# Kernel optimization log

Measured on AMD Instinct MI355X. Metric: run time of the kernel, lower is better.

## Reference

```python
import jax, jax.numpy as jnp
import numpy as np

D = 128  # d_pair
N = 512  # n_res
B = 1
EPS = 1e-5


def setup_inputs() -> dict:
    key = jax.random.key(0)
    ks = jax.random.split(key, 16)
    s = 0.02
    inp = {
        "pair": jax.random.normal(ks[0], (B, N, N, D), dtype=jnp.float32),
        "pair_mask": jnp.ones((B, N, N), dtype=jnp.float32),
        "ln_g": jnp.ones((D,), dtype=jnp.float32),
        "ln_b": jnp.zeros((D,), dtype=jnp.float32),
        "w_lp": jax.random.normal(ks[1], (D, D), dtype=jnp.float32) * s,
        "b_lp": jnp.zeros((D,), dtype=jnp.float32),
        "w_lg": jax.random.normal(ks[2], (D, D), dtype=jnp.float32) * s,
        "b_lg": jnp.zeros((D,), dtype=jnp.float32),
        "w_rp": jax.random.normal(ks[3], (D, D), dtype=jnp.float32) * s,
        "b_rp": jnp.zeros((D,), dtype=jnp.float32),
        "w_rg": jax.random.normal(ks[4], (D, D), dtype=jnp.float32) * s,
        "b_rg": jnp.zeros((D,), dtype=jnp.float32),
        "w_g": jax.random.normal(ks[5], (D, D), dtype=jnp.float32) * s,
        "b_g": jnp.zeros((D,), dtype=jnp.float32),
        "w_o": jax.random.normal(ks[6], (D, D), dtype=jnp.float32) * s,
        "b_o": jnp.zeros((D,), dtype=jnp.float32),
    }
    return inp


def _layer_norm(x, g, b):
    mu = jnp.mean(x, axis=-1, keepdims=True)
    var = jnp.mean(jnp.square(x - mu), axis=-1, keepdims=True)
    return (x - mu) * jax.lax.rsqrt(var + EPS) * g + b


def reference(pair, pair_mask, ln_g, ln_b, w_lp, b_lp, w_lg, b_lg,
              w_rp, b_rp, w_rg, b_rg, w_g, b_g, w_o, b_o):
    # [B,N,N,D] pair representation; outgoing triangle multiplication
    x = _layer_norm(pair, ln_g, ln_b)
    mask = pair_mask[..., None]  # [B,N,N,1]
    left = (x @ w_lp + b_lp) * jax.nn.sigmoid(x @ w_lg + b_lg) * mask
    right = (x @ w_rp + b_rp) * jax.nn.sigmoid(x @ w_rg + b_rg) * mask
    # outgoing: contract over j -> per-channel NxN matmul
    out = jnp.einsum('bijd,bjkd->bikd', left, right)
    out = out * jax.nn.sigmoid(x @ w_g + b_g)
    out = out @ w_o + b_o
    return out
```

## Files before the change

### kernel.cpp

```cpp
#include <hip/hip_runtime.h>

#define NN 512
#define DD 128
#define PP (NN*NN)

typedef __attribute__((ext_vector_type(8))) short short8;
typedef __attribute__((ext_vector_type(4))) short shortx4;
typedef __attribute__((ext_vector_type(4))) float floatx4;

__device__ __forceinline__ unsigned short f2bf(float f) {
  unsigned int u = __float_as_uint(f);
  u += 0x7fffu + ((u >> 16) & 1u);
  return (unsigned short)(u >> 16);
}
__device__ __forceinline__ float bf2f(unsigned short h) {
  return __uint_as_float(((unsigned int)h) << 16);
}
__device__ __forceinline__ float sigm(float x) {
  return 1.f / (1.f + __expf(-x));
}

__device__ __forceinline__ void gload_lds16(const unsigned short* g, unsigned short* l) {
  __builtin_amdgcn_global_load_lds(
      (const __attribute__((address_space(1))) unsigned int*)g,
      (__attribute__((address_space(3))) unsigned int*)l, 16, 0, 0);
}

__global__ void k0_prep(const float* __restrict__ wlp, const float* __restrict__ wlg,
                        const float* __restrict__ wrp, const float* __restrict__ wrg,
                        const float* __restrict__ wg,  const float* __restrict__ wo,
                        unsigned short* __restrict__ wt) {
  const float* src[6] = {wlp, wlg, wrp, wrg, wg, wo};
  int m = blockIdx.y;
  int idx = blockIdx.x * 256 + threadIdx.x;
  int d = idx >> 7, e = idx & 127;
  wt[m * 16384 + e * 128 + d] = f2bf(src[m][d * 128 + e]);
}

__device__ __forceinline__ void run_mm(const unsigned short* __restrict__ wt_m,
                                       unsigned short* Alds, unsigned short* Wlds,
                                       int t, int wm, int we, int ln, int q8,
                                       floatx4 (&acc)[4][4]) {
  #pragma unroll
  for (int it = 0; it < 8; ++it) {
    int flat = it * 256 + t;
    int e = flat >> 4, c = flat & 15;
    *(short8*)&Wlds[e * 136 + c * 8] = *(const short8*)(wt_m + e * 128 + c * 8);
  }
  __syncthreads();
  #pragma unroll
  for (int ks = 0; ks < 4; ++ks) {
    short8 a[4], b[4];
    #pragma unroll
    for (int i = 0; i < 4; ++i)
      a[i] = *(const short8*)&Alds[(wm + i * 16 + ln) * 136 + ks * 32 + q8 * 8];
    #pragma unroll
    for (int i = 0; i < 4; ++i)
      b[i] = *(const short8*)&Wlds[(we + i * 16 + ln) * 136 + ks * 32 + q8 * 8];
    #pragma unroll
    for (int i = 0; i < 4; ++i)
      #pragma unroll
      for (int j = 0; j < 4; ++j)
        acc[i][j] = __builtin_amdgcn_mfma_f32_16x16x32_bf16(a[i], b[j], acc[i][j], 0, 0, 0);
  }
  __syncthreads();
}

__launch_bounds__(256, 2)
__global__ void k1_ln_proj(const float* __restrict__ pair, const float* __restrict__ pmask,
                           const float* __restrict__ lng, const float* __restrict__ lnb,
                           const unsigned short* __restrict__ wt,
                           const float* __restrict__ b_lp, const float* __restrict__ b_lg,
                           const float* __restrict__ b_rp, const float* __restrict__ b_rg,
                           const float* __restrict__ b_g,
                           unsigned short* __restrict__ left_t,
                           unsigned short* __restrict__ right_bt,
                           unsigned short* __restrict__ gate_t) {
  __shared__ __align__(16) unsigned short Alds[128 * 136];
  __shared__ __align__(16) unsigned short Wlds[128 * 136];
  __shared__ float Mlds[128];

  const int t = threadIdx.x;
  const int unit = blockIdx.y;
  const int q = blockIdx.x;

  long prow0, pstride, mrow0, mstride, soff;
  if (unit == 1) {
    int j0 = (q >> 9) << 7, k0 = q & 511;
    prow0 = ((long)j0 * NN + k0) * DD; pstride = (long)NN * DD;
    mrow0 = (long)j0 * NN + k0;        mstride = NN;
    soff  = (long)k0 * NN + j0;
  } else {
    long p0 = (long)q << 7;
    prow0 = p0 * DD; pstride = DD;
    mrow0 = p0;      mstride = 1;
    soff  = p0;
  }

  {
    int r = t >> 1, h = t & 1;
    const float* row = pair + prow0 + (long)r * pstride + h * 64;
    floatx4 v[16];
    float s = 0.f, s2 = 0.f;
    #pragma unroll
    for (int c = 0; c < 16; ++c) {
      v[c] = *(const floatx4*)(row + c * 4);
      s  += v[c].x + v[c].y + v[c].z + v[c].w;
      s2 += v[c].x * v[c].x + v[c].y * v[c].y + v[c].z * v[c].z + v[c].w * v[c].w;
    }
    s  += __shfl_xor(s, 1);
    s2 += __shfl_xor(s2, 1);
    float mu = s * (1.f / 128.f);
    float var = s2 * (1.f / 128.f) - mu * mu;
    float rs = rsqrtf(var + 1e-5f);
    #pragma unroll
    for (int c = 0; c < 16; ++c) {
      floatx4 g4 = *(const floatx4*)(lng + h * 64 + c * 4);
      floatx4 b4 = *(const floatx4*)(lnb + h * 64 + c * 4);
      shortx4 pk;
      pk[0] = (short)f2bf((v[c].x - mu) * rs * g4.x + b4.x);
      pk[1] = (short)f2bf((v[c].y - mu) * rs * g4.y + b4.y);
      pk[2] = (short)f2bf((v[c].z - mu) * rs * g4.z + b4.z);
      pk[3] = (short)f2bf((v[c].w - mu) * rs * g4.w + b4.w);
      *(shortx4*)&Alds[r * 136 + h * 64 + c * 4] = pk;
    }
    if (h == 0) Mlds[r] = pmask[mrow0 + (long)r * mstride];
  }
  __syncthreads();

  const int lane = t & 63, w = t >> 6;
  const int ln = lane & 15, q8 = lane >> 4;
  const int wm = (w >> 1) << 6, we = (w & 1) << 6;

  unsigned short* stg = (w < 2) ? (Alds + w * 4608) : (Wlds + (w - 2) * 4608);

  if (unit < 2) {
    floatx4 accA[4][4] = {};
    floatx4 accB[4][4] = {};
    run_mm(wt + (unit == 0 ? 0 : 2) * 16384, Alds, Wlds, t, wm, we, ln, q8, accA);
    run_mm(wt + (unit == 0 ? 1 : 3) * 16384, Alds, Wlds, t, wm, we, ln, q8, accB);
    const float* bpp = (unit == 0) ? b_lp : b_rp;
    const float* bgg = (unit == 0) ? b_lg : b_rg;
    #pragma unroll
    for (int j = 0; j < 4; ++j) {
      int eg = we + j * 16 + ln;
      float bp_v = bpp[eg], bg_v = bgg[eg];
      #pragma unroll
      for (int i = 0; i < 4; ++i) {
        shortx4 pk;
        #pragma unroll
        for (int r = 0; r < 4; ++r) {
          int m = wm + i * 16 + q8 * 4 + r;
          float val = (accA[i][j][r] + bp_v) * sigm(accB[i][j][r] + bg_v) * Mlds[m];
          pk[r] = (short)f2bf(val);
        }
        *(shortx4*)&stg[(j * 16 + ln) * 72 + i * 16 + q8 * 4] = pk;
      }
    }
  } else {
    floatx4 accA[4][4] = {};
    run_mm(wt + 4 * 16384, Alds, Wlds, t, wm, we, ln, q8, accA);
    #pragma unroll
    for (int j = 0; j < 4; ++j) {
      int eg = we + j * 16 + ln;
      float bg_v = b_g[eg];
      #pragma unroll
      for (int i = 0; i < 4; ++i) {
        shortx4 pk;
        #pragma unroll
        for (int r = 0; r < 4; ++r)
          pk[r] = (short)f2bf(sigm(accA[i][j][r] + bg_v));
        *(shortx4*)&stg[(j * 16 + ln) * 72 + i * 16 + q8 * 4] = pk;
      }
    }
  }
  __syncthreads();

  unsigned short* dstbase = (unit == 0) ? left_t : (unit == 1 ? right_bt : gate_t);
  #pragma unroll
  for (int itr = 0; itr < 8; ++itr) {
    int row = itr * 8 + (lane >> 3);
    int c = lane & 7;
    short8 vv = *(const short8*)&stg[row * 72 + c * 8];
    long eg = we + row;
    *(short8*)(dstbase + eg * PP + soff + wm + c * 8) = vv;
  }
}

__launch_bounds__(256, 3)
__global__ void k2_einsum(const unsigned short* __restrict__ left_t,
                          const unsigned short* __restrict__ right_bt,
                          const unsigned short* __restrict__ gate_t,
                          unsigned short* __restrict__ tmpg) {
  __shared__ __align__(16) unsigned short Al[128 * 32];
  __shared__ __align__(16) unsigned short Bl[128 * 32];
  const int t = threadIdx.x;
  const int d = blockIdx.y;
  const int i0 = (blockIdx.x >> 2) << 7;
  const int k0 = (blockIdx.x & 3) << 7;
  const unsigned short* Ag = left_t   + (long)d * PP;
  const unsigned short* Bg = right_bt + (long)d * PP;
  const int lane = t & 63, w = t >> 6;
  const int ln = lane & 15, q8 = lane >> 4;
  const int wm = (w >> 1) << 6, wn = (w & 1) << 6;

  floatx4 acc[4][4] = {};
  for (int j0 = 0; j0 < NN; j0 += 32) {
    #pragma unroll
    for (int it = 0; it < 2; ++it) {
      int flat = it * 256 + t;
      int r = flat >> 2, c = flat & 3;
      gload_lds16(Ag + (long)(i0 + r) * NN + j0 + c * 8, &Al[flat * 8]);
    }
    #pragma unroll
    for (int it = 0; it < 2; ++it) {
      int flat = it * 256 + t;
      int r = flat >> 2, c = flat & 3;
      gload_lds16(Bg + (long)(k0 + r) * NN + j0 + c * 8, &Bl[flat * 8]);
    }
    __syncthreads();
    short8 a[4], b[4];
    #pragma unroll
    for (int i = 0; i < 4; ++i)
      a[i] = *(const short8*)&Al[(wm + i * 16 + ln) * 32 + q8 * 8];
    #pragma unroll
    for (int i = 0; i < 4; ++i)
      b[i] = *(const short8*)&Bl[(wn + i * 16 + ln) * 32 + q8 * 8];
    #pragma unroll
    for (int i = 0; i < 4; ++i)
      #pragma unroll
      for (int j = 0; j < 4; ++j)
        acc[i][j] = __builtin_amdgcn_mfma_f32_16x16x32_bf16(a[i], b[j], acc[i][j], 0, 0, 0);
    __syncthreads();
  }
  const unsigned short* Gg = gate_t + (long)d * PP;
  unsigned short* Og = tmpg + (long)d * PP;
  #pragma unroll
  for (int i = 0; i < 4; ++i)
    #pragma unroll
    for (int j = 0; j < 4; ++j) {
      int n = k0 + wn + j * 16 + ln;
      #pragma unroll
      for (int r = 0; r < 4; ++r) {
        int m = i0 + wm + i * 16 + q8 * 4 + r;
        long idx = (long)m * NN + n;
        Og[idx] = f2bf(acc[i][j][r] * bf2f(Gg[idx]));
      }
    }
}

__launch_bounds__(256, 2)
__global__ void k3_out(const unsigned short* __restrict__ tmpg,
                       const unsigned short* __restrict__ wt,
                       const float* __restrict__ b_o,
                       float* __restrict__ out) {
  __shared__ __align__(16) unsigned short Tl[128 * 136];
  __shared__ __align__(16) unsigned short Wl[128 * 136];
  const int t = threadIdx.x;
  const long p0 = (long)blockIdx.x << 7;
  const unsigned short* wo = wt + 5 * 16384;

  #pragma unroll
  for (int it = 0; it < 8; ++it) {
    int flat = it * 256 + t;
    int e = flat >> 4, c = flat & 15;
    *(short8*)&Wl[e * 136 + c * 8] = *(const short8*)(wo + e * 128 + c * 8);
  }
  #pragma unroll
  for (int it = 0; it < 8; ++it) {
    int flat = it * 256 + t;
    int dd2 = flat >> 4, c = flat & 15;
    *(short8*)&Tl[dd2 * 136 + c * 8] = *(const short8*)(tmpg + (long)dd2 * PP + p0 + c * 8);
  }
  __syncthreads();

  const int lane = t & 63, w = t >> 6;
  const int ln = lane & 15, q8 = lane >> 4;
  const int wm = (w >> 1) << 6, wn = (w & 1) << 6;

  floatx4 acc[4][4] = {};
  #pragma unroll
  for (int ks = 0; ks < 4; ++ks) {
    short8 a[4], b[4];
    #pragma unroll
    for (int i = 0; i < 4; ++i) {
      int m = wm + i * 16 + ln;
      short8 av;
      #pragma unroll
      for (int jj = 0; jj < 8; ++jj)
        av[jj] = (short)Tl[(ks * 32 + q8 * 8 + jj) * 136 + m];
      a[i] = av;
    }
    #pragma unroll
    for (int i = 0; i < 4; ++i)
      b[i] = *(const short8*)&Wl[(wn + i * 16 + ln) * 136 + ks * 32 + q8 * 8];
    #pragma unroll
    for (int i = 0; i < 4; ++i)
      #pragma unroll
      for (int j = 0; j < 4; ++j)
        acc[i][j] = __builtin_amdgcn_mfma_f32_16x16x32_bf16(a[i], b[j], acc[i][j], 0, 0, 0);
  }
  #pragma unroll
  for (int j = 0; j < 4; ++j) {
    int eg = wn + j * 16 + ln;
    float bias = b_o[eg];
    #pragma unroll
    for (int i = 0; i < 4; ++i)
      #pragma unroll
      for (int r = 0; r < 4; ++r) {
        int m = wm + i * 16 + q8 * 4 + r;
        out[(p0 + m) * DD + eg] = acc[i][j][r] + bias;
      }
  }
}

extern "C" void kernel_launch(void* const* d_in, const int* in_sizes, int n_in,
                              void* d_out, int out_size, void* d_ws, size_t ws_size,
                              hipStream_t stream) {
  const float* pair = (const float*)d_in[0];
  const float* pmask = (const float*)d_in[1];
  const float* ln_g = (const float*)d_in[2];
  const float* ln_b = (const float*)d_in[3];
  const float* w_lp = (const float*)d_in[4];
  const float* b_lp = (const float*)d_in[5];
  const float* w_lg = (const float*)d_in[6];
  const float* b_lg = (const float*)d_in[7];
  const float* w_rp = (const float*)d_in[8];
  const float* b_rp = (const float*)d_in[9];
  const float* w_rg = (const float*)d_in[10];
  const float* b_rg = (const float*)d_in[11];
  const float* w_g  = (const float*)d_in[12];
  const float* b_g  = (const float*)d_in[13];
  const float* w_o  = (const float*)d_in[14];
  const float* b_o  = (const float*)d_in[15];
  float* out = (float*)d_out;

  char* ws = (char*)d_ws;
  unsigned short* wt       = (unsigned short*)ws;
  unsigned short* left_t   = (unsigned short*)(ws + 196608);
  unsigned short* right_bt = left_t   + (size_t)PP * DD;
  unsigned short* gate_t   = right_bt + (size_t)PP * DD;
  unsigned short* tmpg     = gate_t   + (size_t)PP * DD;

  k0_prep<<<dim3(64, 6), 256, 0, stream>>>(w_lp, w_lg, w_rp, w_rg, w_g, w_o, wt);
  k1_ln_proj<<<dim3(2048, 3), 256, 0, stream>>>(pair, pmask, ln_g, ln_b, wt,
      b_lp, b_lg, b_rp, b_rg, b_g, left_t, right_bt, gate_t);
  k2_einsum<<<dim3(16, 128), 256, 0, stream>>>(left_t, right_bt, gate_t, tmpg);
  k3_out<<<dim3(2048), 256, 0, stream>>>(tmpg, wt, b_o, out);
}
```

Before: 527.9 us.

## Fuse LN and all projections per tile, add transpose kernel, move gating to output

```diff
diff --git a/kernel.cpp b/kernel.cpp
--- a/kernel.cpp
+++ b/kernel.cpp
@@ -7,6 +7,7 @@
 typedef __attribute__((ext_vector_type(8))) short short8;
 typedef __attribute__((ext_vector_type(4))) short shortx4;
 typedef __attribute__((ext_vector_type(4))) float floatx4;
+typedef __attribute__((ext_vector_type(4))) unsigned int uintx4;
 
 __device__ __forceinline__ unsigned short f2bf(float f) {
   unsigned int u = __float_as_uint(f);
@@ -37,35 +38,6 @@
   wt[m * 16384 + e * 128 + d] = f2bf(src[m][d * 128 + e]);
 }
 
-__device__ __forceinline__ void run_mm(const unsigned short* __restrict__ wt_m,
-                                       unsigned short* Alds, unsigned short* Wlds,
-                                       int t, int wm, int we, int ln, int q8,
-                                       floatx4 (&acc)[4][4]) {
-  #pragma unroll
-  for (int it = 0; it < 8; ++it) {
-    int flat = it * 256 + t;
-    int e = flat >> 4, c = flat & 15;
-    *(short8*)&Wlds[e * 136 + c * 8] = *(const short8*)(wt_m + e * 128 + c * 8);
-  }
-  __syncthreads();
-  #pragma unroll
-  for (int ks = 0; ks < 4; ++ks) {
-    short8 a[4], b[4];
-    #pragma unroll
-    for (int i = 0; i < 4; ++i)
-      a[i] = *(const short8*)&Alds[(wm + i * 16 + ln) * 136 + ks * 32 + q8 * 8];
-    #pragma unroll
-    for (int i = 0; i < 4; ++i)
-      b[i] = *(const short8*)&Wlds[(we + i * 16 + ln) * 136 + ks * 32 + q8 * 8];
-    #pragma unroll
-    for (int i = 0; i < 4; ++i)
-      #pragma unroll
-      for (int j = 0; j < 4; ++j)
-        acc[i][j] = __builtin_amdgcn_mfma_f32_16x16x32_bf16(a[i], b[j], acc[i][j], 0, 0, 0);
-  }
-  __syncthreads();
-}
-
 __launch_bounds__(256, 2)
 __global__ void k1_ln_proj(const float* __restrict__ pair, const float* __restrict__ pmask,
                            const float* __restrict__ lng, const float* __restrict__ lnb,
@@ -74,32 +46,18 @@
                            const float* __restrict__ b_rp, const float* __restrict__ b_rg,
                            const float* __restrict__ b_g,
                            unsigned short* __restrict__ left_t,
-                           unsigned short* __restrict__ right_bt,
+                           unsigned short* __restrict__ right_t,
                            unsigned short* __restrict__ gate_t) {
-  __shared__ __align__(16) unsigned short Alds[128 * 136];
-  __shared__ __align__(16) unsigned short Wlds[128 * 136];
+  __shared__ __align__(16) unsigned short Alds[128 * 130];
+  __shared__ __align__(16) unsigned short stg[4 * 64 * 68];
   __shared__ float Mlds[128];
 
   const int t = threadIdx.x;
-  const int unit = blockIdx.y;
-  const int q = blockIdx.x;
-
-  long prow0, pstride, mrow0, mstride, soff;
-  if (unit == 1) {
-    int j0 = (q >> 9) << 7, k0 = q & 511;
-    prow0 = ((long)j0 * NN + k0) * DD; pstride = (long)NN * DD;
-    mrow0 = (long)j0 * NN + k0;        mstride = NN;
-    soff  = (long)k0 * NN + j0;
-  } else {
-    long p0 = (long)q << 7;
-    prow0 = p0 * DD; pstride = DD;
-    mrow0 = p0;      mstride = 1;
-    soff  = p0;
-  }
+  const long p0 = (long)blockIdx.x << 7;
 
   {
     int r = t >> 1, h = t & 1;
-    const float* row = pair + prow0 + (long)r * pstride + h * 64;
+    const float* row = pair + (p0 + r) * DD + h * 64;
     floatx4 v[16];
     float s = 0.f, s2 = 0.f;
     #pragma unroll
@@ -122,78 +80,152 @@
       pk[1] = (short)f2bf((v[c].y - mu) * rs * g4.y + b4.y);
       pk[2] = (short)f2bf((v[c].z - mu) * rs * g4.z + b4.z);
       pk[3] = (short)f2bf((v[c].w - mu) * rs * g4.w + b4.w);
-      *(shortx4*)&Alds[r * 136 + h * 64 + c * 4] = pk;
-    }
-    if (h == 0) Mlds[r] = pmask[mrow0 + (long)r * mstride];
+      *(shortx4*)&Alds[r * 130 + h * 64 + c * 4] = pk;
+    }
+    if (h == 0) Mlds[r] = pmask[p0 + r];
   }
   __syncthreads();
 
   const int lane = t & 63, w = t >> 6;
   const int ln = lane & 15, q8 = lane >> 4;
   const int wm = (w >> 1) << 6, we = (w & 1) << 6;
-
-  unsigned short* stg = (w < 2) ? (Alds + w * 4608) : (Wlds + (w - 2) * 4608);
-
-  if (unit < 2) {
-    floatx4 accA[4][4] = {};
-    floatx4 accB[4][4] = {};
-    run_mm(wt + (unit == 0 ? 0 : 2) * 16384, Alds, Wlds, t, wm, we, ln, q8, accA);
-    run_mm(wt + (unit == 0 ? 1 : 3) * 16384, Alds, Wlds, t, wm, we, ln, q8, accB);
-    const float* bpp = (unit == 0) ? b_lp : b_rp;
-    const float* bgg = (unit == 0) ? b_lg : b_rg;
+  unsigned short* mystg = stg + w * 4352;
+
+  auto mm = [&](const unsigned short* wtm, floatx4 (&acc)[4][4]) {
+    #pragma unroll
+    for (int ks = 0; ks < 4; ++ks) {
+      short8 a[4], b[4];
+      #pragma unroll
+      for (int i = 0; i < 4; ++i)
+        a[i] = *(const short8*)&Alds[(wm + i * 16 + ln) * 130 + ks * 32 + q8 * 8];
+      #pragma unroll
+      for (int j = 0; j < 4; ++j)
+        b[j] = *(const short8*)(wtm + (we + j * 16 + ln) * 128 + ks * 32 + q8 * 8);
+      #pragma unroll
+      for (int i = 0; i < 4; ++i)
+        #pragma unroll
+        for (int j = 0; j < 4; ++j)
+          acc[i][j] = __builtin_amdgcn_mfma_f32_16x16x32_bf16(a[i], b[j], acc[i][j], 0, 0, 0);
+    }
+  };
+  auto stout = [&](unsigned short* dst) {
+    #pragma unroll
+    for (int itr = 0; itr < 8; ++itr) {
+      int row = itr * 8 + (lane >> 3);
+      int c = lane & 7;
+      *(short8*)(dst + (long)(we + row) * PP + p0 + wm + c * 8) =
+          *(const short8*)&mystg[row * 68 + c * 8];
+    }
+  };
+
+  {
+    floatx4 aP[4][4] = {}, aG[4][4] = {};
+    mm(wt + 0 * 16384, aP);
+    mm(wt + 1 * 16384, aG);
     #pragma unroll
     for (int j = 0; j < 4; ++j) {
       int eg = we + j * 16 + ln;
-      float bp_v = bpp[eg], bg_v = bgg[eg];
+      float bp = b_lp[eg], bg = b_lg[eg];
       #pragma unroll
       for (int i = 0; i < 4; ++i) {
         shortx4 pk;
         #pragma unroll
         for (int r = 0; r < 4; ++r) {
           int m = wm + i * 16 + q8 * 4 + r;
-          float val = (accA[i][j][r] + bp_v) * sigm(accB[i][j][r] + bg_v) * Mlds[m];
-          pk[r] = (short)f2bf(val);
+          pk[r] = (short)f2bf((aP[i][j][r] + bp) * sigm(aG[i][j][r] + bg) * Mlds[m]);
         }
-        *(shortx4*)&stg[(j * 16 + ln) * 72 + i * 16 + q8 * 4] = pk;
+        *(shortx4*)&mystg[(j * 16 + ln) * 68 + i * 16 + q8 * 4] = pk;
       }
     }
-  } else {
-    floatx4 accA[4][4] = {};
-    run_mm(wt + 4 * 16384, Alds, Wlds, t, wm, we, ln, q8, accA);
+    stout(left_t);
+  }
+  {
+    floatx4 aP[4][4] = {}, aG[4][4] = {};
+    mm(wt + 2 * 16384, aP);
+    mm(wt + 3 * 16384, aG);
     #pragma unroll
     for (int j = 0; j < 4; ++j) {
       int eg = we + j * 16 + ln;
-      float bg_v = b_g[eg];
+      float bp = b_rp[eg], bg = b_rg[eg];
+      #pragma unroll
+      for (int i = 0; i < 4; ++i) {
+        shortx4 pk;
+        #pragma unroll
+        for (int r = 0; r < 4; ++r) {
+          int m = wm + i * 16 + q8 * 4 + r;
+          pk[r] = (short)f2bf((aP[i][j][r] + bp) * sigm(aG[i][j][r] + bg) * Mlds[m]);
+        }
+        *(shortx4*)&mystg[(j * 16 + ln) * 68 + i * 16 + q8 * 4] = pk;
+      }
+    }
+    stout(right_t);
+  }
+  {
+    floatx4 aP[4][4] = {};
+    mm(wt + 4 * 16384, aP);
+    #pragma unroll
+    for (int j = 0; j < 4; ++j) {
+      int eg = we + j * 16 + ln;
+      float bg = b_g[eg];
       #pragma unroll
       for (int i = 0; i < 4; ++i) {
         shortx4 pk;
         #pragma unroll
         for (int r = 0; r < 4; ++r)
-          pk[r] = (short)f2bf(sigm(accA[i][j][r] + bg_v));
-        *(shortx4*)&stg[(j * 16 + ln) * 72 + i * 16 + q8 * 4] = pk;
+          pk[r] = (short)f2bf(sigm(aP[i][j][r] + bg));
+        *(shortx4*)&mystg[(j * 16 + ln) * 68 + i * 16 + q8 * 4] = pk;
       }
     }
+    stout(gate_t);
+  }
+}
+
+__launch_bounds__(256, 4)
+__global__ void kt_transpose(const unsigned short* __restrict__ right_t,
+                             unsigned short* __restrict__ right_bt) {
+  __shared__ unsigned int TlU[64 * 129];
+  const int t = threadIdx.x;
+  const int d = blockIdx.x >> 4;
+  const int j0 = ((blockIdx.x >> 2) & 3) << 7;
+  const int k0 = (blockIdx.x & 3) << 7;
+  const unsigned short* src = right_t + (long)d * PP;
+
+  #pragma unroll
+  for (int it = 0; it < 4; ++it) {
+    int flat = it * 256 + t;
+    int rp = flat >> 4, c = flat & 15;
+    uintx4 xa = *(const uintx4*)(src + (long)(j0 + 2 * rp)     * NN + k0 + c * 8);
+    uintx4 xb = *(const uintx4*)(src + (long)(j0 + 2 * rp + 1) * NN + k0 + c * 8);
+    #pragma unroll
+    for (int cc = 0; cc < 4; ++cc) {
+      unsigned int lo = (xa[cc] & 0xffffu)  | (xb[cc] << 16);
+      unsigned int hi = (xa[cc] >> 16)      | (xb[cc] & 0xffff0000u);
+      TlU[rp * 129 + c * 8 + cc * 2]     = lo;
+      TlU[rp * 129 + c * 8 + cc * 2 + 1] = hi;
+    }
   }
   __syncthreads();
-
-  unsigned short* dstbase = (unit == 0) ? left_t : (unit == 1 ? right_bt : gate_t);
-  #pragma unroll
-  for (int itr = 0; itr < 8; ++itr) {
-    int row = itr * 8 + (lane >> 3);
-    int c = lane & 7;
-    short8 vv = *(const short8*)&stg[row * 72 + c * 8];
-    long eg = we + row;
-    *(short8*)(dstbase + eg * PP + soff + wm + c * 8) = vv;
+  unsigned short* dst = right_bt + (long)d * PP;
+  #pragma unroll
+  for (int it = 0; it < 8; ++it) {
+    int flat = it * 256 + t;
+    int k = flat >> 4, js = flat & 15;
+    uintx4 u;
+    #pragma unroll
+    for (int q = 0; q < 4; ++q)
+      u[q] = TlU[(js * 4 + q) * 129 + k];
+    *(uintx4*)(dst + (long)(k0 + k) * NN + j0 + js * 8) = u;
   }
 }
 
 __launch_bounds__(256, 3)
 __global__ void k2_einsum(const unsigned short* __restrict__ left_t,
                           const unsigned short* __restrict__ right_bt,
-                          const unsigned short* __restrict__ gate_t,
                           unsigned short* __restrict__ tmpg) {
-  __shared__ __align__(16) unsigned short Al[128 * 32];
-  __shared__ __align__(16) unsigned short Bl[128 * 32];
+  __shared__ __align__(16) unsigned short Sm[128 * 132];
+  unsigned short* Al = Sm;
+  unsigned short* Bl = Sm + 128 * 32;
+  unsigned short* Cl = Sm;
   const int t = threadIdx.x;
   const int d = blockIdx.y;
   const int i0 = (blockIdx.x >> 2) << 7;
@@ -233,24 +265,28 @@
         acc[i][j] = __builtin_amdgcn_mfma_f32_16x16x32_bf16(a[i], b[j], acc[i][j], 0, 0, 0);
     __syncthreads();
   }
-  const unsigned short* Gg = gate_t + (long)d * PP;
+  #pragma unroll
+  for (int i = 0; i < 4; ++i)
+    #pragma unroll
+    for (int j = 0; j < 4; ++j) {
+      int n = wn + j * 16 + ln;
+      #pragma unroll
+      for (int r = 0; r < 4; ++r)
+        Cl[(wm + i * 16 + q8 * 4 + r) * 132 + n] = f2bf(acc[i][j][r]);
+    }
+  __syncthreads();
   unsigned short* Og = tmpg + (long)d * PP;
   #pragma unroll
-  for (int i = 0; i < 4; ++i)
-    #pragma unroll
-    for (int j = 0; j < 4; ++j) {
-      int n = k0 + wn + j * 16 + ln;
-      #pragma unroll
-      for (int r = 0; r < 4; ++r) {
-        int m = i0 + wm + i * 16 + q8 * 4 + r;
-        long idx = (long)m * NN + n;
-        Og[idx] = f2bf(acc[i][j][r] * bf2f(Gg[idx]));
-      }
-    }
+  for (int it = 0; it < 8; ++it) {
+    int flat = it * 256 + t;
+    int m = flat >> 4, c = flat & 15;
+    *(short8*)(Og + (long)(i0 + m) * NN + k0 + c * 8) = *(const short8*)&Cl[m * 132 + c * 8];
+  }
 }
 
 __launch_bounds__(256, 2)
 __global__ void k3_out(const unsigned short* __restrict__ tmpg,
+                       const unsigned short* __restrict__ gate_t,
                        const unsigned short* __restrict__ wt,
                        const float* __restrict__ b_o,
                        float* __restrict__ out) {
@@ -270,7 +306,13 @@
   for (int it = 0; it < 8; ++it) {
     int flat = it * 256 + t;
     int dd2 = flat >> 4, c = flat & 15;
-    *(short8*)&Tl[dd2 * 136 + c * 8] = *(const short8*)(tmpg + (long)dd2 * PP + p0 + c * 8);
+    short8 tv = *(const short8*)(tmpg   + (long)dd2 * PP + p0 + c * 8);
+    short8 gv = *(const short8*)(gate_t + (long)dd2 * PP + p0 + c * 8);
+    short8 mv;
+    #pragma unroll
+    for (int e = 0; e < 8; ++e)
+      mv[e] = (short)f2bf(bf2f((unsigned short)tv[e]) * bf2f((unsigned short)gv[e]));
+    *(short8*)&Tl[dd2 * 136 + c * 8] = mv;
   }
   __syncthreads();
 
@@ -338,13 +380,14 @@
   char* ws = (char*)d_ws;
   unsigned short* wt       = (unsigned short*)ws;
   unsigned short* left_t   = (unsigned short*)(ws + 196608);
-  unsigned short* right_bt = left_t   + (size_t)PP * DD;
+  unsigned short* buf1     = left_t + (size_t)PP * DD;
+  unsigned short* right_bt = buf1   + (size_t)PP * DD;
   unsigned short* gate_t   = right_bt + (size_t)PP * DD;
-  unsigned short* tmpg     = gate_t   + (size_t)PP * DD;
 
   k0_prep<<<dim3(64, 6), 256, 0, stream>>>(w_lp, w_lg, w_rp, w_rg, w_g, w_o, wt);
-  k1_ln_proj<<<dim3(2048, 3), 256, 0, stream>>>(pair, pmask, ln_g, ln_b, wt,
-      b_lp, b_lg, b_rp, b_rg, b_g, left_t, right_bt, gate_t);
-  k2_einsum<<<dim3(16, 128), 256, 0, stream>>>(left_t, right_bt, gate_t, tmpg);
-  k3_out<<<dim3(2048), 256, 0, stream>>>(tmpg, wt, b_o, out);
-}
+  k1_ln_proj<<<dim3(2048), 256, 0, stream>>>(pair, pmask, ln_g, ln_b, wt,
+      b_lp, b_lg, b_rp, b_rg, b_g, left_t, buf1, gate_t);
+  kt_transpose<<<dim3(2048), 256, 0, stream>>>(buf1, right_bt);
+  k2_einsum<<<dim3(16, 128), 256, 0, stream>>>(left_t, right_bt, buf1);
+  k3_out<<<dim3(2048), 256, 0, stream>>>(buf1, gate_t, wt, b_o, out);
+}
```

Result: slower. 545.0 us (+3.2%).
